# Kernel optimization log

Hardware: AMD Instinct MI355X
Metric: run time of the kernel (lower is better)

Reference implementation:

```python
import jax, jax.numpy as jnp
import numpy as np

KNN = 10        # knn init arg
FAC = 2.0       # fac init arg
SIGMA = 0.5     # self.sigma (fixed in module)
N, D = 4096, 128


def setup_inputs() -> dict:
    key = jax.random.key(0)
    k1, k2, k3 = jax.random.split(key, 3)
    return {
        "x": jax.random.normal(k1, (N, D), dtype=jnp.float32),
        "alpha": 0.01 * jax.random.normal(k2, (D,), dtype=jnp.float32),
        "base_noise": jax.random.normal(k3, (D,), dtype=jnp.float32),
    }


def _full_affinity_knn(Xm):
    r = jnp.sum(Xm * Xm, axis=1, keepdims=True)          # [N,1]
    Dx = r - 2.0 * (Xm @ Xm.T) + r.T                     # [N,N]
    # full row sort, take (knn-1)-th smallest distance per row
    sorted_d = jnp.sort(Dx, axis=1)                      # [N,N]
    knn_d = sorted_d[:, KNN - 1]                         # [N]
    # calculate_percentiles(percentile=50)
    s = jnp.sort(knn_d)
    n = s.shape[0]
    idx = int(50.0 / 100.0 * n)
    if n % 2 == 0:
        mu, ml = s[idx], s[idx - 1]
    else:
        mu = ml = s[idx]
    sigma = (mu + ml) / 2.0
    sigma = jnp.where(sigma < 1e-8, jnp.float32(1.0), sigma)
    W = jnp.exp(-Dx / (FAC * sigma))                     # [N,N]
    # Dminus @ W == row-normalize (diag matmul replaced by broadcast divide)
    P = W / jnp.sum(W, axis=1, keepdims=True)
    return P


def reference(x, alpha, base_noise):
    # feature_selector: hard_sigmoid(alpha + sigma*noise) applied per-feature
    z = alpha + SIGMA * base_noise
    gate = jnp.clip(z + 0.5, 0.0, 1.0)
    masked = x * gate[None, :]                           # [N,D]
    P = _full_affinity_knn(masked)                       # [N,N]
    return (P, masked)
```

## Files before the change

### kernel.cpp

```cpp
#include <hip/hip_runtime.h>
#include <math.h>

#define NROW 4096
#define NDIM 128
#define KNN 10

typedef __bf16 bf16x8 __attribute__((ext_vector_type(8)));
typedef unsigned short u16x8 __attribute__((ext_vector_type(8)));
typedef float f32x4 __attribute__((ext_vector_type(4)));

__device__ inline unsigned short f2bf(float f) {
    unsigned int u = __float_as_uint(f);
    u += 0x7FFFu + ((u >> 16) & 1u);
    return (unsigned short)(u >> 16);
}
__device__ inline float bf2f(unsigned short u) {
    return __uint_as_float((unsigned)u << 16);
}


__global__ __launch_bounds__(128) void k_mask(const float* __restrict__ x,
                                              const float* __restrict__ alpha,
                                              const float* __restrict__ noise,
                                              float* __restrict__ masked,
                                              unsigned short* __restrict__ mb,
                                              float* __restrict__ r) {
    int row = blockIdx.x;
    int c = threadIdx.x;
    float g = alpha[c] + 0.5f * noise[c] + 0.5f;
    g = fminf(fmaxf(g, 0.0f), 1.0f);
    float m = x[row * NDIM + c] * g;
    masked[row * NDIM + c] = m;
    mb[row * NDIM + c] = f2bf(m);
    float v = m * m;
#pragma unroll
    for (int o = 32; o > 0; o >>= 1) v += __shfl_down(v, o, 64);
    __shared__ float partial[2];
    if ((c & 63) == 0) partial[c >> 6] = v;
    __syncthreads();
    if (c == 0) r[row] = partial[0] + partial[1];
}

__global__ __launch_bounds__(256) void k_dx(const unsigned short* __restrict__ Mb,
                                            const float* __restrict__ r,
                                            float* __restrict__ P) {
    int tid = threadIdx.x;
    int bx = blockIdx.x, by = blockIdx.y;
    int wave = tid >> 6, lane = tid & 63;
    int wr = wave >> 1, wc = wave & 1;
    int quad = lane >> 4, l15 = lane & 15;

    int gi_base = by * 128 + wr * 64;
    int gj_base = bx * 128 + wc * 64;

    const unsigned short* Arow = Mb + (size_t)(gi_base + l15) * NDIM + quad * 8;
    const unsigned short* Brow = Mb + (size_t)(gj_base + l15) * NDIM + quad * 8;

    f32x4 acc[4][4];
#pragma unroll
    for (int i = 0; i < 4; ++i)
#pragma unroll
        for (int j = 0; j < 4; ++j) acc[i][j] = (f32x4)(0.0f);

#pragma unroll
    for (int kk = 0; kk < 128; kk += 32) {
        bf16x8 af[4], bfr[4];
#pragma unroll
        for (int t = 0; t < 4; ++t) {
            af[t] = *(const bf16x8*)(Arow + (size_t)t * 16 * NDIM + kk);
            bfr[t] = *(const bf16x8*)(Brow + (size_t)t * 16 * NDIM + kk);
        }
#pragma unroll
        for (int ti = 0; ti < 4; ++ti)
#pragma unroll
            for (int tj = 0; tj < 4; ++tj)
                acc[ti][tj] = __builtin_amdgcn_mfma_f32_16x16x32_bf16(
                    af[ti], bfr[tj], acc[ti][tj], 0, 0, 0);
    }

    float rrow[4][4], rcol[4];
#pragma unroll
    for (int ti = 0; ti < 4; ++ti)
#pragma unroll
        for (int rg = 0; rg < 4; ++rg)
            rrow[ti][rg] = r[gi_base + ti * 16 + quad * 4 + rg];
#pragma unroll
    for (int tj = 0; tj < 4; ++tj) rcol[tj] = r[gj_base + tj * 16 + l15];
#pragma unroll
    for (int ti = 0; ti < 4; ++ti)
#pragma unroll
        for (int rg = 0; rg < 4; ++rg) {
            int grow = gi_base + ti * 16 + quad * 4 + rg;
            __bf16* brow = (__bf16*)(P + (size_t)grow * NROW + NROW / 2);
#pragma unroll
            for (int tj = 0; tj < 4; ++tj) {
                int gcol = gj_base + tj * 16 + l15;
                float d = rrow[ti][rg] + rcol[tj] - 2.0f * acc[ti][tj][rg];
                ((unsigned short*)brow)[gcol] = f2bf(d);
            }
        }
}

__global__ __launch_bounds__(256) void k_knn(const float* __restrict__ P,
                                             float* __restrict__ knn) {
    int tid = threadIdx.x;
    int wave = tid >> 6, lane = tid & 63;
    int row = blockIdx.x * 4 + wave;
    const unsigned short* drow =
        (const unsigned short*)(P + (size_t)row * NROW + NROW / 2);

    float t[KNN];
#pragma unroll
    for (int j = 0; j < KNN; ++j) t[j] = INFINITY;

#pragma unroll
    for (int c = 0; c < 8; ++c) {
        u16x8 v8 = *(const u16x8*)(drow + (c * 64 + lane) * 8);
#pragma unroll
        for (int e = 0; e < 8; ++e) {
            float cv = bf2f(v8[e]);
#pragma unroll
            for (int j = 0; j < KNN; ++j) {
                float lo = fminf(t[j], cv);
                cv = fmaxf(t[j], cv);
                t[j] = lo;
            }
        }
    }

#pragma unroll
    for (int r = 0; r < KNN; ++r) {
        float v = t[0];
        int src = lane;
#pragma unroll
        for (int o = 1; o < 64; o <<= 1) {
            float ov = __shfl_xor(v, o, 64);
            int osrc = __shfl_xor(src, o, 64);
            if (ov < v || (ov == v && osrc < src)) { v = ov; src = osrc; }
        }
        if (r == KNN - 1) {
            if (lane == 0) knn[row] = v;
        } else if (src == lane) {
#pragma unroll
            for (int j = 0; j < KNN - 1; ++j) t[j] = t[j + 1];
            t[KNN - 1] = INFINITY;
        }
    }
}

__device__ inline unsigned fmap(float f) {
    unsigned b = __float_as_uint(f);
    return b ^ ((b >> 31) ? 0xFFFFFFFFu : 0x80000000u);
}
__device__ inline float funmap(unsigned u) {
    unsigned b = (u & 0x80000000u) ? (u ^ 0x80000000u) : ~u;
    return __uint_as_float(b);
}

__global__ __launch_bounds__(1024) void k_sigma(const float* __restrict__ knn,
                                                float* __restrict__ scale_out) {
    __shared__ unsigned keys[NROW];
    __shared__ unsigned hist[2048];
    __shared__ unsigned s_prefix, s_R;
    __shared__ float red_f[16];
    __shared__ unsigned red_u[16];
    int tid = threadIdx.x;
    if (tid == 0) { s_prefix = 0; s_R = 2047; }
#pragma unroll
    for (int l = 0; l < 4; ++l) keys[tid + l * 1024] = fmap(knn[tid + l * 1024]);
    __syncthreads();

    const int shifts[3] = {21, 10, 0};
    const int widths[3] = {11, 11, 10};
    for (int rd = 0; rd < 3; ++rd) {
        int sh = shifts[rd], w = widths[rd];
        unsigned nb = 1u << w;
        hist[tid] = 0;
        hist[tid + 1024] = 0;
        __syncthreads();
        unsigned prefix = s_prefix;
        unsigned R = s_R;
        int hsh = sh + w;
#pragma unroll
        for (int l = 0; l < 4; ++l) {
            unsigned k = keys[tid + l * 1024];
            bool match = (rd == 0) || ((k >> hsh) == prefix);
            if (match) atomicAdd(&hist[(k >> sh) & (nb - 1u)], 1u);
        }
        __syncthreads();
        if (tid < 64) {
            unsigned chunk = nb >> 6;
            unsigned base = tid * chunk;
            unsigned lsum = 0;
            for (unsigned i = 0; i < chunk; ++i) lsum += hist[base + i];
            unsigned pfx = lsum;
#pragma unroll
            for (int o = 1; o < 64; o <<= 1) {
                unsigned v = __shfl_up(pfx, o, 64);
                if (tid >= o) pfx += v;
            }
            unsigned excl = pfx - lsum;
            if (R >= excl && R < excl + lsum) {
                unsigned cum = excl;
                for (unsigned i = 0; i < chunk; ++i) {
                    unsigned h = hist[base + i];
                    if (R < cum + h) {
                        s_prefix = (prefix << w) | (base + i);
                        s_R = R - cum;
                        break;
                    }
                    cum += h;
                }
            }
        }
        __syncthreads();
    }

    unsigned mlk = s_prefix;
    unsigned cnt = 0, mng = 0xFFFFFFFFu;
#pragma unroll
    for (int l = 0; l < 4; ++l) {
        unsigned k = keys[tid + l * 1024];
        if (k <= mlk) cnt++;
        else mng = min(mng, k);
    }
#pragma unroll
    for (int o = 32; o > 0; o >>= 1) {
        cnt += __shfl_down(cnt, o, 64);
        mng = min(mng, (unsigned)__shfl_down(mng, o, 64));
    }
    int lane = tid & 63, wid = tid >> 6;
    if (lane == 0) { red_u[wid] = cnt; red_f[wid] = __uint_as_float(mng); }
    __syncthreads();
    if (tid == 0) {
        unsigned ctot = 0, m = 0xFFFFFFFFu;
        for (int w = 0; w < 16; ++w) {
            ctot += red_u[w];
            m = min(m, __float_as_uint(red_f[w]));
        }
        float ml = funmap(mlk);
        float mu = (ctot >= 2049u) ? ml : funmap(m);
        float sigma = 0.5f * (mu + ml);
        if (sigma < 1e-8f) sigma = 1.0f;
        scale_out[0] = -1.0f / (2.0f * sigma);
    }
}

__global__ __launch_bounds__(256) void k_norm(float* __restrict__ P,
                                              const float* __restrict__ scale_p) {
    int row = blockIdx.x, tid = threadIdx.x;
    float scale = scale_p[0];
    float* drow = P + (size_t)row * NROW;
    const unsigned short* brow = (const unsigned short*)(drow + NROW / 2);

    u16x8 a = *(const u16x8*)(brow + tid * 16);
    u16x8 b = *(const u16x8*)(brow + tid * 16 + 8);
    float v[16];
#pragma unroll
    for (int e = 0; e < 8; ++e) v[e] = __expf(bf2f(a[e]) * scale);
#pragma unroll
    for (int e = 0; e < 8; ++e) v[8 + e] = __expf(bf2f(b[e]) * scale);
    float sum = 0.0f;
#pragma unroll
    for (int e = 0; e < 16; ++e) sum += v[e];
#pragma unroll
    for (int o = 32; o > 0; o >>= 1) sum += __shfl_down(sum, o, 64);
    __shared__ float ps[4];
    int lane = tid & 63, wid = tid >> 6;
    if (lane == 0) ps[wid] = sum;
    __syncthreads();
    float inv = 1.0f / (ps[0] + ps[1] + ps[2] + ps[3]);
#pragma unroll
    for (int l = 0; l < 4; ++l) {
        float4 o4;
        o4.x = v[l * 4 + 0] * inv;
        o4.y = v[l * 4 + 1] * inv;
        o4.z = v[l * 4 + 2] * inv;
        o4.w = v[l * 4 + 3] * inv;
        *(float4*)(drow + tid * 16 + l * 4) = o4;
    }
}

extern "C" void kernel_launch(void* const* d_in, const int* in_sizes, int n_in,
                              void* d_out, int out_size, void* d_ws, size_t ws_size,
                              hipStream_t stream) {
    const float* x = (const float*)d_in[0];
    const float* alpha = (const float*)d_in[1];
    const float* noise = (const float*)d_in[2];
    float* out = (float*)d_out;
    float* P = out;
    float* masked = out + (size_t)NROW * NROW;
    float* ws = (float*)d_ws;
    float* r = ws;
    float* knn = ws + NROW;
    float* scale = ws + 2 * NROW;
    unsigned short* Mb = (unsigned short*)(ws + 3 * NROW);

    k_mask<<<NROW, 128, 0, stream>>>(x, alpha, noise, masked, Mb, r);
    k_dx<<<dim3(NROW / 128, NROW / 128), 256, 0, stream>>>(Mb, r, P);
    k_knn<<<NROW / 4, 256, 0, stream>>>(P, knn);
    k_sigma<<<1, 1024, 0, stream>>>(knn, scale);
    k_norm<<<NROW, 256, 0, stream>>>(P, scale);
}
```

Measured before the change: 153.6 us.

## Exploit distance-matrix symmetry with upper-triangular tiles and LDS-staged operands

The distance kernel now launches only the upper-triangular 128x128 tiles (528 blocks instead of 1024) and writes each off-diagonal result twice, once as is and once transposed, using the symmetry of X X^T. Operand tiles are staged into padded shared memory with coalesced 16-byte loads rather than each wave loading fragments straight from global memory. This halves the MFMA work and operand loads. In exchange, the mirrored bf16 stores are scattered 2-byte writes along columns, which are poorly coalesced and may cost more than the compute saved.

```diff
diff --git a/kernel.cpp b/kernel.cpp
--- a/kernel.cpp
+++ b/kernel.cpp
@@ -4,6 +4,7 @@
 #define NROW 4096
 #define NDIM 128
 #define KNN 10
+#define LDSS 136
 
 typedef __bf16 bf16x8 __attribute__((ext_vector_type(8)));
 typedef unsigned short u16x8 __attribute__((ext_vector_type(8)));
@@ -44,18 +45,33 @@
 __global__ __launch_bounds__(256) void k_dx(const unsigned short* __restrict__ Mb,
                                             const float* __restrict__ r,
                                             float* __restrict__ P) {
+    __shared__ __align__(16) __bf16 Asm[128 * LDSS];
+    __shared__ __align__(16) __bf16 Bsm[128 * LDSS];
     int tid = threadIdx.x;
-    int bx = blockIdx.x, by = blockIdx.y;
+
+    int bid = blockIdx.x;
+    int by = 0, rem = bid;
+    while (rem >= 32 - by) { rem -= 32 - by; ++by; }
+    int bx = by + rem;
+
+    {
+        const unsigned short* Ap = Mb + (size_t)by * 128 * NDIM;
+        const unsigned short* Bp = Mb + (size_t)bx * 128 * NDIM;
+        int c = (tid & 15) * 8;
+        int r0 = tid >> 4;
+#pragma unroll
+        for (int i = 0; i < 8; ++i) {
+            int row = r0 + i * 16;
+            *(uint4*)&Asm[row * LDSS + c] = *(const uint4*)(Ap + row * NDIM + c);
+            *(uint4*)&Bsm[row * LDSS + c] = *(const uint4*)(Bp + row * NDIM + c);
+        }
+    }
+    __syncthreads();
+
     int wave = tid >> 6, lane = tid & 63;
     int wr = wave >> 1, wc = wave & 1;
     int quad = lane >> 4, l15 = lane & 15;
 
-    int gi_base = by * 128 + wr * 64;
-    int gj_base = bx * 128 + wc * 64;
-
-    const unsigned short* Arow = Mb + (size_t)(gi_base + l15) * NDIM + quad * 8;
-    const unsigned short* Brow = Mb + (size_t)(gj_base + l15) * NDIM + quad * 8;
-
     f32x4 acc[4][4];
 #pragma unroll
     for (int i = 0; i < 4; ++i)
@@ -64,12 +80,14 @@
 
 #pragma unroll
     for (int kk = 0; kk < 128; kk += 32) {
+        int ka = kk + quad * 8;
         bf16x8 af[4], bfr[4];
 #pragma unroll
-        for (int t = 0; t < 4; ++t) {
-            af[t] = *(const bf16x8*)(Arow + (size_t)t * 16 * NDIM + kk);
-            bfr[t] = *(const bf16x8*)(Brow + (size_t)t * 16 * NDIM + kk);
-        }
+        for (int ti = 0; ti < 4; ++ti)
+            af[ti] = *(const bf16x8*)&Asm[(wr * 64 + ti * 16 + l15) * LDSS + ka];
+#pragma unroll
+        for (int tj = 0; tj < 4; ++tj)
+            bfr[tj] = *(const bf16x8*)&Bsm[(wc * 64 + tj * 16 + l15) * LDSS + ka];
 #pragma unroll
         for (int ti = 0; ti < 4; ++ti)
 #pragma unroll
@@ -78,6 +96,8 @@
                     af[ti], bfr[tj], acc[ti][tj], 0, 0, 0);
     }
 
+    int gi_base = by * 128 + wr * 64;
+    int gj_base = bx * 128 + wc * 64;
     float rrow[4][4], rcol[4];
 #pragma unroll
     for (int ti = 0; ti < 4; ++ti)
@@ -86,17 +106,26 @@
             rrow[ti][rg] = r[gi_base + ti * 16 + quad * 4 + rg];
 #pragma unroll
     for (int tj = 0; tj < 4; ++tj) rcol[tj] = r[gj_base + tj * 16 + l15];
+
+    bool mirror = (bx != by);
 #pragma unroll
     for (int ti = 0; ti < 4; ++ti)
 #pragma unroll
         for (int rg = 0; rg < 4; ++rg) {
             int grow = gi_base + ti * 16 + quad * 4 + rg;
-            __bf16* brow = (__bf16*)(P + (size_t)grow * NROW + NROW / 2);
+            unsigned short* brow =
+                (unsigned short*)(P + (size_t)grow * NROW + NROW / 2);
 #pragma unroll
             for (int tj = 0; tj < 4; ++tj) {
                 int gcol = gj_base + tj * 16 + l15;
                 float d = rrow[ti][rg] + rcol[tj] - 2.0f * acc[ti][tj][rg];
-                ((unsigned short*)brow)[gcol] = f2bf(d);
+                unsigned short db = f2bf(d);
+                brow[gcol] = db;
+                if (mirror) {
+                    unsigned short* bcol =
+                        (unsigned short*)(P + (size_t)gcol * NROW + NROW / 2);
+                    bcol[grow] = db;
+                }
             }
         }
 }
@@ -297,7 +326,7 @@
     unsigned short* Mb = (unsigned short*)(ws + 3 * NROW);
 
     k_mask<<<NROW, 128, 0, stream>>>(x, alpha, noise, masked, Mb, r);
-    k_dx<<<dim3(NROW / 128, NROW / 128), 256, 0, stream>>>(Mb, r, P);
+    k_dx<<<528, 256, 0, stream>>>(Mb, r, P);
     k_knn<<<NROW / 4, 256, 0, stream>>>(P, knn);
     k_sigma<<<1, 1024, 0, stream>>>(knn, scale);
     k_norm<<<NROW, 256, 0, stream>>>(P, scale);
```

Measured after the change: 161.7 us. 5.3% more time.
